# Optimization experiments

Measured on AMD Instinct MI355X. Metric: run time of the kernel, lower is better.

The kernel has to match this reference:

```python
import jax, jax.numpy as jnp
import numpy as np

B, T, D, H = 4, 2048, 1024, 16
HD = D // H  # head_dim = 64


def setup_inputs() -> dict:
    key = jax.random.key(0)
    k1, k2, k3 = jax.random.split(key, 3)
    x = jax.random.normal(k1, (B, T, D), dtype=jnp.float32)
    # torch Linear weights: [out_features, in_features], kaiming-ish scale
    Wqkv = jax.random.normal(k2, (3 * D, D), dtype=jnp.float32) * (1.0 / np.sqrt(D))
    Wout = jax.random.normal(k3, (D, D), dtype=jnp.float32) * (1.0 / np.sqrt(D))
    return {"x": x, "Wqkv": Wqkv, "Wout": Wout}


def reference(x, Wqkv, Wout):
    b, t, c = x.shape
    qkv = x @ Wqkv.T                      # [B,T,3D]
    q, k, v = jnp.split(qkv, 3, axis=2)
    # [B,T,D] -> [B,H,T,HD]
    q = q.reshape(b, t, H, HD).transpose(0, 2, 1, 3)
    k = k.reshape(b, t, H, HD).transpose(0, 2, 1, 3)
    v = v.reshape(b, t, H, HD).transpose(0, 2, 1, 3)
    scale = 1.0 / np.sqrt(HD).astype(np.float32)
    att = jnp.einsum('bhqd,bhkd->bhqk', q, k) * scale  # [B,H,T,T]
    causal = jnp.tril(jnp.ones((t, t), dtype=bool))
    att = jnp.where(causal[None, None], att, -jnp.inf)
    att = jax.nn.softmax(att, axis=-1)
    y = jnp.einsum('bhqk,bhkd->bhqd', att, v)          # [B,H,T,HD]
    y = y.transpose(0, 2, 1, 3).reshape(b, t, c)       # [B,T,D]
    return y @ Wout.T
```

## Files before the change

kernel.cpp:

```cpp
#include <hip/hip_runtime.h>
#include <hip/hip_bf16.h>
#include <stdint.h>

#define B_ 4
#define T_ 2048
#define D_ 1024
#define H_ 16
#define M_ (B_*T_)
#define N1_ (3*D_)

typedef __attribute__((ext_vector_type(8))) short short8;
typedef __attribute__((ext_vector_type(4))) short short4v;
typedef __attribute__((ext_vector_type(4))) float f32x4;
typedef __attribute__((ext_vector_type(16))) float f32x16;

typedef const __attribute__((address_space(1))) void* as1cp;
typedef __attribute__((address_space(3))) void* as3p;

__device__ __forceinline__ ushort f2bf(float f) {
  union { float f; unsigned u; } v; v.f = f;
  unsigned r = v.u + 0x7fffu + ((v.u >> 16) & 1u);
  return (ushort)(r >> 16);
}

__global__ void cast3_f32_bf16(const float* __restrict__ a, ushort* __restrict__ oa, int na,
                               const float* __restrict__ b, ushort* __restrict__ ob, int nb,
                               const float* __restrict__ c, ushort* __restrict__ oc, int nc) {
  int i = blockIdx.x * blockDim.x + threadIdx.x;
  int stride = gridDim.x * blockDim.x;
  int ntot = na + nb + nc;
  for (; i < ntot; i += stride) {
    const float* src; ushort* dst; int j = i;
    if (j < na) { src = a; dst = oa; }
    else if ((j -= na) < nb) { src = b; dst = ob; }
    else { j -= nb; src = c; dst = oc; }
    float4 v = reinterpret_cast<const float4*>(src)[j];
    ushort4 o;
    o.x = f2bf(v.x); o.y = f2bf(v.y); o.z = f2bf(v.z); o.w = f2bf(v.w);
    reinterpret_cast<ushort4*>(dst)[j] = o;
  }
}

__device__ __forceinline__ void gload_lds16(const ushort* g, ushort* l) {
  __builtin_amdgcn_global_load_lds((as1cp)(const void*)g, (as3p)(void*)l, 16, 0, 0);
}

__device__ __forceinline__ short4v ds_tr16(unsigned addr) {
  short4v r;
  asm volatile("ds_read_b64_tr_b16 %0, %1" : "=v"(r) : "v"(addr) : "memory");
  return r;
}

__device__ __forceinline__ short8 cat8(short4v a, short4v b) {
  short8 r;
  r[0]=a[0]; r[1]=a[1]; r[2]=a[2]; r[3]=a[3];
  r[4]=b[0]; r[5]=b[1]; r[6]=b[2]; r[7]=b[3];
  return r;
}

__device__ __forceinline__ unsigned cvtpk(float lo, float hi) {
  unsigned r;
  asm("v_cvt_pk_bf16_f32 %0, %1, %2" : "=v"(r) : "v"(lo), "v"(hi));
  return r;
}

__device__ __forceinline__ f32x16 mfma32(short8 a, short8 b, f32x16 c) {
  return __builtin_amdgcn_mfma_f32_32x32x16_bf16(a, b, c, 0, 0, 0);
}

template<int MODE>
__global__ __launch_bounds__(256) void gemm_bt(const ushort* __restrict__ A,
                                               const ushort* __restrict__ Bm,
                                               void* __restrict__ Cout,
                                               int M, int N, int K, int gx) {
  __shared__ ushort Al[128*32];
  __shared__ ushort Bl[128*32];
  const int tid  = threadIdx.x;
  const int lane = tid & 63;
  const int w    = tid >> 6;
  const int g    = lane >> 4;
  const int ln   = lane & 15;

  const int nwg = gridDim.x;
  const int cpx = nwg >> 3;
  const int id  = (int)blockIdx.x;
  const int swz = (id & 7) * cpx + (id >> 3);
  const int m0 = (swz / gx) * 128;
  const int n0 = (swz % gx) * 128;
  const int wr = w >> 1, wc = w & 1;

  f32x4 acc[4][4] = {};

  for (int kt = 0; kt < K; kt += 32) {
    __syncthreads();
    #pragma unroll
    for (int j = 0; j < 2; ++j) {
      int cc  = w * 2 + j;
      int idx = cc * 64 + lane;
      int row = idx >> 2;
      int kofs = (idx & 3) * 8;
      gload_lds16(A  + (size_t)(m0 + row) * K + kt + kofs, &Al[cc * 512]);
      gload_lds16(Bm + (size_t)(n0 + row) * K + kt + kofs, &Bl[cc * 512]);
    }
    __syncthreads();
    short8 a[4], b[4];
    #pragma unroll
    for (int m = 0; m < 4; ++m)
      a[m] = *(const short8*)&Al[(wr*64 + m*16 + ln) * 32 + g*8];
    #pragma unroll
    for (int n = 0; n < 4; ++n)
      b[n] = *(const short8*)&Bl[(wc*64 + n*16 + ln) * 32 + g*8];
    #pragma unroll
    for (int m = 0; m < 4; ++m)
      #pragma unroll
      for (int n = 0; n < 4; ++n)
        acc[m][n] = __builtin_amdgcn_mfma_f32_16x16x32_bf16(a[m], b[n], acc[m][n], 0, 0, 0);
  }

  #pragma unroll
  for (int m = 0; m < 4; ++m) {
    int gr = m0 + wr*64 + m*16 + g*4;
    #pragma unroll
    for (int n = 0; n < 4; ++n) {
      int gc = n0 + wc*64 + n*16 + ln;
      #pragma unroll
      for (int r = 0; r < 4; ++r) {
        float v = acc[m][n][r];
        if (MODE == 2 && gc < 1024) v *= 0.18033688011112042f;
        if (MODE) ((ushort*)Cout)[(size_t)(gr + r) * N + gc] = f2bf(v);
        else      ((float*)Cout)[(size_t)(gr + r) * N + gc]  = v;
      }
    }
  }
}

__global__ __launch_bounds__(512, 2) void attn9(const ushort* __restrict__ qkv,
                                                ushort* __restrict__ y) {
  __shared__ ushort Kl[2][8192];
  __shared__ ushort Vl[2][8192];

  const int tid  = threadIdx.x;
  const int lane = tid & 63;
  const int w    = tid >> 6;
  const int l31  = lane & 31;
  const int hi   = lane >> 5;

  const int bh = blockIdx.x;
  const int b  = bh >> 4;
  const int h  = bh & 15;
  const int qb = 7 - (int)blockIdx.y;
  const int rowg = b * T_;
  const int q0 = qb * 256;
  const int qw = q0 + w * 32;
  const int qrow = qw + l31;
  const int nt = 2 * qb + 2;

  const int krow0 = tid >> 3;
  const int kcb   = ((tid & 7) * 16) ^ ((krow0 & 7) << 4);
  const int vdh = tid & 1, vr = (tid >> 1) & 3, vg = (tid >> 3) & 3,
            vkq = (tid >> 5) & 1, vks = (tid >> 6) & 7;
  const int vkey = vks*16 + vkq*8 + (vg >> 1)*4 + vr;
  const int vdd  = (vg & 1)*16 + vdh*8;

  short8 qf[4];
  {
    const ushort* qp = qkv + (size_t)(rowg + qrow) * N1_ + h*64 + hi*8;
    #pragma unroll
    for (int kc = 0; kc < 4; ++kc) qf[kc] = *(const short8*)(qp + kc*16);
  }

  f32x16 oacc[2] = {};
  float lrun = 0.f;

  const unsigned VbBase = (unsigned)(size_t)(as3p)(void*)&Vl[0][0];
  const unsigned trln = (unsigned)(((lane >> 4) * 128) + (lane & 15) * 8);

  auto STAGE = [&](int bufi, int kb) {
    const ushort* Ks = qkv + (size_t)(rowg + kb + krow0) * N1_ + D_ + h*64 + (kcb >> 1);
    gload_lds16(Ks,                     &Kl[bufi][tid*8]);
    gload_lds16(Ks + (size_t)64 * N1_,  &Kl[bufi][(512 + tid)*8]);
    const ushort* Vs = qkv + (size_t)(rowg + kb + vkey) * N1_ + 2*D_ + h*64 + vdd;
    gload_lds16(Vs,      &Vl[bufi][tid*8]);
    gload_lds16(Vs + 32, &Vl[bufi][(512 + tid)*8]);
  };

  STAGE(0, 0);

  for (int kt = 0; kt < nt; ++kt) {
    const int buf = kt & 1;
    const int kbase = kt * 128;
    if (kt + 1 < nt) {
      STAGE(buf ^ 1, kbase + 128);
      asm volatile("s_waitcnt vmcnt(4)" ::: "memory");
    } else {
      asm volatile("s_waitcnt vmcnt(0)" ::: "memory");
    }
    asm volatile("s_barrier" ::: "memory");

    #pragma unroll
    for (int h2 = 0; h2 < 2; ++h2) {
      const int kb2 = kbase + h2 * 64;
      if (kb2 <= qw + 31) {
        f32x16 sv[2] = {};
        const char* Kb = (const char*)&Kl[buf][0] + h2 * 8192;
        __builtin_amdgcn_s_setprio(1);
        #pragma unroll
        for (int kc = 0; kc < 4; ++kc) {
          unsigned co = (unsigned)((kc*32 + hi*16) ^ ((l31 & 7) << 4));
          short8 k0 = *(const short8*)(Kb + (size_t)l31*128 + co);
          short8 k1 = *(const short8*)(Kb + (size_t)(32 + l31)*128 + co);
          sv[0] = mfma32(k0, qf[kc], sv[0]);
          sv[1] = mfma32(k1, qf[kc], sv[1]);
        }
        __builtin_amdgcn_s_setprio(0);

        if (kb2 + 63 > qw) {
          #pragma unroll
          for (int t = 0; t < 2; ++t)
            #pragma unroll
            for (int r = 0; r < 16; ++r) {
              int kl = kb2 + t*32 + (r & 3) + 8*(r >> 2) + 4*hi;
              if (kl > qrow) sv[t][r] = -1.0e38f;
            }
        }

        #pragma unroll
        for (int t = 0; t < 2; ++t)
          #pragma unroll
          for (int r = 0; r < 16; ++r) sv[t][r] = exp2f(sv[t][r] - 12.0f);
        float ts[8];
        #pragma unroll
        for (int r = 0; r < 8; ++r)
          ts[r] = (sv[0][r] + sv[0][r+8]) + (sv[1][r] + sv[1][r+8]);
        lrun += ((ts[0] + ts[1]) + (ts[2] + ts[3])) + ((ts[4] + ts[5]) + (ts[6] + ts[7]));

        const unsigned Vb = VbBase + (unsigned)(buf * 16384);
        short4v vt[2][4][2];
        #pragma unroll
        for (int dt = 0; dt < 2; ++dt)
          #pragma unroll
          for (int ks = 0; ks < 4; ++ks) {
            unsigned a = Vb + (unsigned)(dt*8192 + (h2*4 + ks)*1024) + trln;
            vt[dt][ks][0] = ds_tr16(a);
            vt[dt][ks][1] = ds_tr16(a + 512);
          }

        short8 pa[4];
        #pragma unroll
        for (int ks = 0; ks < 4; ++ks) {
          const int t = ks >> 1, base = 8 * (ks & 1);
          union { unsigned u[4]; short8 v; } uu;
          uu.u[0] = cvtpk(sv[t][base+0], sv[t][base+1]);
          uu.u[1] = cvtpk(sv[t][base+2], sv[t][base+3]);
          uu.u[2] = cvtpk(sv[t][base+4], sv[t][base+5]);
          uu.u[3] = cvtpk(sv[t][base+6], sv[t][base+7]);
          pa[ks] = uu.v;
        }

        asm volatile("s_waitcnt lgkmcnt(0)" ::: "memory");
        __builtin_amdgcn_sched_barrier(0);
        __builtin_amdgcn_s_setprio(1);
        #pragma unroll
        for (int ks = 0; ks < 4; ++ks) {
          oacc[0] = mfma32(cat8(vt[0][ks][0], vt[0][ks][1]), pa[ks], oacc[0]);
          oacc[1] = mfma32(cat8(vt[1][ks][0], vt[1][ks][1]), pa[ks], oacc[1]);
        }
        __builtin_amdgcn_s_setprio(0);
      }
    }
    asm volatile("s_barrier" ::: "memory");
  }

  float ltot = lrun + __shfl_xor(lrun, 32);
  const float inv = 1.0f / ltot;
  #pragma unroll
  for (int dt = 0; dt < 2; ++dt) {
    #pragma unroll
    for (int rq = 0; rq < 4; ++rq) {
      ushort4 pk4;
      pk4.x = f2bf(oacc[dt][rq*4+0] * inv);
      pk4.y = f2bf(oacc[dt][rq*4+1] * inv);
      pk4.z = f2bf(oacc[dt][rq*4+2] * inv);
      pk4.w = f2bf(oacc[dt][rq*4+3] * inv);
      *(ushort4*)&y[(size_t)(rowg + qrow) * D_ + h*64 + dt*32 + rq*8 + hi*4] = pk4;
    }
  }
}

extern "C" void kernel_launch(void* const* d_in, const int* in_sizes, int n_in,
                              void* d_out, int out_size, void* d_ws, size_t ws_size,
                              hipStream_t stream) {
  const float* x    = (const float*)d_in[0];
  const float* Wqkv = (const float*)d_in[1];
  const float* Wout = (const float*)d_in[2];

  ushort* xb    = (ushort*)d_ws;
  ushort* wqkvb = xb    + (size_t)M_ * D_;
  ushort* woutb = wqkvb + (size_t)N1_ * D_;
  ushort* qkvb  = woutb + (size_t)D_ * D_;
  ushort* yb    = qkvb  + (size_t)M_ * N1_;

  cast3_f32_bf16<<<2048, 256, 0, stream>>>(x, xb, M_ * D_ / 4,
                                           Wqkv, wqkvb, N1_ * D_ / 4,
                                           Wout, woutb, D_ * D_ / 4);

  gemm_bt<2><<<(N1_/128)*(M_/128), 256, 0, stream>>>(xb, wqkvb, qkvb, M_, N1_, D_, N1_/128);

  attn9<<<dim3(B_*H_, 8), 512, 0, stream>>>(qkvb, yb);

  gemm_bt<0><<<(D_/128)*(M_/128), 256, 0, stream>>>(yb, woutb, d_out, M_, D_, D_, D_/128);
}
```

Measured before the change: 186.4 us.

## Use 256x256-tile 8-wave GEMM with XCD swizzle for QKV projection

Adds a new bf16 GEMM kernel that uses 256x256 output tiles with 512 threads, double-buffered direct-to-LDS loads, an XCD-aware block swizzle and phased MFMA issue with priority hints, and uses it for the QKV projection. Larger tiles raise arithmetic intensity and cut global/L2 traffic compared with the 128x128 kernel. The cost is heavier register and LDS use (128 KB LDS per block with launch bounds of 2), which lowers occupancy, and extra barriers inside each K step.

```diff
diff --git a/kernel.cpp b/kernel.cpp
--- a/kernel.cpp
+++ b/kernel.cpp
@@ -134,6 +134,109 @@
   }
 }
 
+template<int MODE>
+__global__ __launch_bounds__(512, 2) void gemm8p(const ushort* __restrict__ A,
+                                                 const ushort* __restrict__ Bm,
+                                                 void* __restrict__ Cout,
+                                                 int M, int N, int K, int gx) {
+  __shared__ ushort lds[2][32768];
+  const int tid  = threadIdx.x;
+  const int lane = tid & 63;
+  const int w    = tid >> 6;
+  const int wr   = w >> 2;
+  const int wc   = w & 3;
+  const int l15  = lane & 15;
+  const int lk   = lane >> 4;
+
+  const int nwg = gridDim.x;
+  const int cpx = nwg >> 3;
+  const int id  = (int)blockIdx.x;
+  const int swz = (id & 7) * cpx + (id >> 3);
+  const int m0 = (swz / gx) * 256;
+  const int n0 = (swz % gx) * 256;
+
+  int srow[4], sk[4];
+  #pragma unroll
+  for (int j = 0; j < 4; ++j) {
+    int f = j * 8 + w;
+    srow[j] = (f >> 4) * 128 + ((f & 15) >> 1) * 16 + l15;
+    sk[j]   = (f & 1) * 32 + lk * 8;
+  }
+
+  const int NT = K >> 6;
+
+  auto STAGE = [&](int slot, int t) {
+    const int k0 = t << 6;
+    #pragma unroll
+    for (int j = 0; j < 4; ++j)
+      gload_lds16(A  + (size_t)(m0 + srow[j]) * K + k0 + sk[j], &lds[slot][j*4096 + w*512]);
+    #pragma unroll
+    for (int j = 0; j < 4; ++j)
+      gload_lds16(Bm + (size_t)(n0 + srow[j]) * K + k0 + sk[j], &lds[slot][16384 + j*4096 + w*512]);
+  };
+
+  f32x4 acc[8][4] = {};
+
+  STAGE(0, 0);
+  STAGE(1, 1);
+
+  for (int it = 0; it < NT; ++it) {
+    const int slot = it & 1;
+    if (it + 1 < NT) asm volatile("s_waitcnt vmcnt(8)" ::: "memory");
+    else             asm volatile("s_waitcnt vmcnt(0)" ::: "memory");
+    asm volatile("s_barrier" ::: "memory");
+
+    const ushort* As = &lds[slot][wr * 8192];
+    const ushort* Bs = &lds[slot][16384 + (wc >> 1) * 8192];
+    const int bfb = (wc & 1) * 4;
+
+    #pragma unroll
+    for (int ph = 0; ph < 4; ++ph) {
+      const int mq = ph >> 1, nh = ph & 1;
+      short8 af[4][2], bf[2][2];
+      #pragma unroll
+      for (int i = 0; i < 4; ++i)
+        #pragma unroll
+        for (int kh = 0; kh < 2; ++kh)
+          af[i][kh] = *(const short8*)&As[((mq*4 + i)*2 + kh)*512 + lane*8];
+      #pragma unroll
+      for (int j2 = 0; j2 < 2; ++j2)
+        #pragma unroll
+        for (int kh = 0; kh < 2; ++kh)
+          bf[j2][kh] = *(const short8*)&Bs[((bfb + nh*2 + j2)*2 + kh)*512 + lane*8];
+      __builtin_amdgcn_s_setprio(1);
+      #pragma unroll
+      for (int i = 0; i < 4; ++i)
+        #pragma unroll
+        for (int j2 = 0; j2 < 2; ++j2)
+          #pragma unroll
+          for (int kh = 0; kh < 2; ++kh)
+            acc[mq*4+i][nh*2+j2] =
+              __builtin_amdgcn_mfma_f32_16x16x32_bf16(af[i][kh], bf[j2][kh],
+                                                      acc[mq*4+i][nh*2+j2], 0, 0, 0);
+      __builtin_amdgcn_s_setprio(0);
+      asm volatile("s_barrier" ::: "memory");
+    }
+    if (it + 2 < NT) STAGE(slot, it + 2);
+  }
+
+  #pragma unroll
+  for (int fm = 0; fm < 8; ++fm) {
+    const int gr = m0 + wr*128 + fm*16 + lk*4;
+    #pragma unroll
+    for (int fn = 0; fn < 4; ++fn) {
+      const int gc = n0 + wc*64 + fn*16 + l15;
+      #pragma unroll
+      for (int r = 0; r < 4; ++r) {
+        float v = acc[fm][fn][r];
+        if (MODE == 2 && gc < 1024) v *= 0.18033688011112042f;
+        if (MODE) ((ushort*)Cout)[(size_t)(gr + r) * N + gc] = f2bf(v);
+        else      ((float*)Cout)[(size_t)(gr + r) * N + gc]  = v;
+      }
+    }
+  }
+}
+
 __global__ __launch_bounds__(512, 2) void attn9(const ushort* __restrict__ qkv,
                                                 ushort* __restrict__ y) {
   __shared__ ushort Kl[2][8192];
@@ -304,7 +407,7 @@
                                            Wqkv, wqkvb, N1_ * D_ / 4,
                                            Wout, woutb, D_ * D_ / 4);
 
-  gemm_bt<2><<<(N1_/128)*(M_/128), 256, 0, stream>>>(xb, wqkvb, qkvb, M_, N1_, D_, N1_/128);
+  gemm8p<2><<<(M_/256)*(N1_/256), 512, 0, stream>>>(xb, wqkvb, qkvb, M_, N1_, D_, N1_/256);
 
   attn9<<<dim3(B_*H_, 8), 512, 0, stream>>>(qkvb, yb);
 
```

After: 202.7 us. 8.7% more time.
